# Optimization experiments

Measured on AMD Instinct MI355X. Metric: run time of the kernel, lower is better.

Reference implementation:

```python
import jax, jax.numpy as jnp
import numpy as np

N_EMBD = 1024
N_HEAD = 16
HEAD_SIZE = 64
EPS = 1e-5


def _layer_norm(x, gamma, beta, eps=EPS):
    mu = jnp.mean(x, axis=-1, keepdims=True)
    var = jnp.mean(jnp.square(x - mu), axis=-1, keepdims=True)
    return (x - mu) * jax.lax.rsqrt(var + eps) * gamma + beta


def setup_inputs() -> dict:
    key = jax.random.key(0)
    ks = jax.random.split(key, 10)
    C = N_EMBD
    s = 1.0 / np.sqrt(C)
    x = jax.random.normal(ks[0], (4, 2048, C), dtype=jnp.float32)
    Wq = jax.random.normal(ks[1], (C, C), dtype=jnp.float32) * s
    Wk = jax.random.normal(ks[2], (C, C), dtype=jnp.float32) * s
    Wv = jax.random.normal(ks[3], (C, C), dtype=jnp.float32) * s
    Wo = jax.random.normal(ks[4], (C, C), dtype=jnp.float32) * s
    W1 = jax.random.normal(ks[5], (C, 4 * C), dtype=jnp.float32) * s
    b1 = jnp.zeros((4 * C,), dtype=jnp.float32)
    W2 = jax.random.normal(ks[6], (4 * C, C), dtype=jnp.float32) * (1.0 / np.sqrt(4 * C))
    b2 = jnp.zeros((C,), dtype=jnp.float32)
    g1 = jnp.ones((C,), dtype=jnp.float32)
    be1 = jnp.zeros((C,), dtype=jnp.float32)
    g2 = jnp.ones((C,), dtype=jnp.float32)
    be2 = jnp.zeros((C,), dtype=jnp.float32)
    return {"x": x, "Wq": Wq, "Wk": Wk, "Wv": Wv, "Wo": Wo,
            "W1": W1, "b1": b1, "W2": W2, "b2": b2,
            "g1": g1, "be1": be1, "g2": g2, "be2": be2}


def _block(x, Wq, Wk, Wv, Wo, W1, b1, W2, b2, g1, be1, g2, be2):
    B, T, C = x.shape
    H, D = N_HEAD, HEAD_SIZE
    # attention sub-block
    h = _layer_norm(x, g1, be1)
    q = (h @ Wq.T).reshape(B, T, H, D).transpose(0, 2, 1, 3)  # [B,H,T,D]
    k = (h @ Wk.T).reshape(B, T, H, D).transpose(0, 2, 1, 3)
    v = (h @ Wv.T).reshape(B, T, H, D).transpose(0, 2, 1, 3)
    wei = jnp.einsum("bhqd,bhkd->bhqk", q, k) * (D ** -0.5)
    causal = jnp.tril(jnp.ones((T, T), dtype=bool))
    wei = jnp.where(causal, wei, -jnp.inf)
    wei = jax.nn.softmax(wei, axis=-1)
    out = jnp.einsum("bhqk,bhkd->bhqd", wei, v)
    out = out.transpose(0, 2, 1, 3).reshape(B, T, C)
    x = x + out @ Wo.T
    # FFN sub-block (exact erf GELU, matching torch default)
    h2 = _layer_norm(x, g2, be2)
    ff = jax.nn.gelu(h2 @ W1 + b1, approximate=False) @ W2 + b2
    return x + ff


def reference(x, Wq, Wk, Wv, Wo, W1, b1, W2, b2, g1, be1, g2, be2):
    return _block(x, Wq, Wk, Wv, Wo, W1, b1, W2, b2, g1, be1, g2, be2)
```

## Files before the change

kernel.cpp:

```cpp
#include <hip/hip_runtime.h>
#include <cmath>

typedef unsigned short u16;
typedef __attribute__((ext_vector_type(8))) short bf16x8;
typedef __attribute__((ext_vector_type(4))) float f32x4;

#define TT 2048
#define CC 1024
#define BT 8192

__device__ __forceinline__ u16 f2bf(float f) {
  unsigned u = __builtin_bit_cast(unsigned, f);
  u += 0x7fffu + ((u >> 16) & 1u);
  return (u16)(u >> 16);
}

__device__ __forceinline__ float bf2f(u16 u) {
  return __builtin_bit_cast(float, (unsigned)u << 16);
}

__device__ __forceinline__ float gelu_tanh(float v) {
  float u2 = v * (1.595769122f + 0.071354816f * v * v);
  return v / (1.f + __expf(-u2));
}

__device__ __forceinline__ void gload_lds16(const void* g, void* l) {
  __builtin_amdgcn_global_load_lds(
      (const __attribute__((address_space(1))) void*)g,
      (__attribute__((address_space(3))) void*)l, 16, 0, 0);
}


__global__ __launch_bounds__(256) void cvt_kernel(const float* __restrict__ s,
                                                  u16* __restrict__ d) {
  int i = (blockIdx.x * 256 + threadIdx.x) * 4;
  float4 v = *(const float4*)(s + i);
  ushort4 o;
  o.x = f2bf(v.x); o.y = f2bf(v.y); o.z = f2bf(v.z); o.w = f2bf(v.w);
  *(ushort4*)(d + i) = o;
}

__global__ __launch_bounds__(256) void transpose_cvt(const float* __restrict__ src,
                                                     u16* __restrict__ dst,
                                                     int R, int C) {
  __shared__ float tile[32][33];
  int c0 = blockIdx.x * 32, r0 = blockIdx.y * 32;
  int tx = threadIdx.x, ty = threadIdx.y;
#pragma unroll
  for (int j = 0; j < 4; ++j)
    tile[ty + j * 8][tx] = src[(size_t)(r0 + ty + j * 8) * C + c0 + tx];
  __syncthreads();
#pragma unroll
  for (int j = 0; j < 4; ++j)
    dst[(size_t)(c0 + ty + j * 8) * R + r0 + tx] = f2bf(tile[tx][ty + j * 8]);
}


__global__ __launch_bounds__(256) void ln_kernel(const float* __restrict__ x,
                                                 const float* __restrict__ gw,
                                                 const float* __restrict__ bw,
                                                 u16* __restrict__ out) {
  int row = blockIdx.x;
  int tid = threadIdx.x;
  const size_t base = (size_t)row * CC;
  float4 v = *(const float4*)(x + base + tid * 4);
  float s = v.x + v.y + v.z + v.w;
  float q = v.x * v.x + v.y * v.y + v.z * v.z + v.w * v.w;
#pragma unroll
  for (int o = 32; o > 0; o >>= 1) {
    s += __shfl_down(s, o, 64);
    q += __shfl_down(q, o, 64);
  }
  __shared__ float red[8];
  __shared__ float stat[2];
  int lane = tid & 63, wid = tid >> 6;
  if (!lane) { red[wid] = s; red[4 + wid] = q; }
  __syncthreads();
  if (!tid) {
    float S = red[0] + red[1] + red[2] + red[3];
    float Q = red[4] + red[5] + red[6] + red[7];
    float mu = S * (1.0f / CC);
    float var = Q * (1.0f / CC) - mu * mu;
    stat[0] = mu;
    stat[1] = rsqrtf(var + 1e-5f);
  }
  __syncthreads();
  float mu = stat[0], rs = stat[1];
  int c = tid * 4;
  float4 gv = *(const float4*)(gw + c);
  float4 bv = *(const float4*)(bw + c);
  ushort4 o;
  o.x = f2bf((v.x - mu) * rs * gv.x + bv.x);
  o.y = f2bf((v.y - mu) * rs * gv.y + bv.y);
  o.z = f2bf((v.z - mu) * rs * gv.z + bv.z);
  o.w = f2bf((v.w - mu) * rs * gv.w + bv.w);
  *(ushort4*)(out + base + c) = o;
}


__global__ __launch_bounds__(256) void rf2_kernel(const u16* __restrict__ p0,
                                                  const u16* __restrict__ p1,
                                                  const float* __restrict__ b2,
                                                  const float* __restrict__ resid,
                                                  float* __restrict__ out) {
  int c = threadIdx.x * 4;
  size_t i = (size_t)blockIdx.x * CC + c;
  ushort4 a = *(const ushort4*)(p0 + i);
  ushort4 b = *(const ushort4*)(p1 + i);
  float4 r = *(const float4*)(resid + i);
  float4 bb = *(const float4*)(b2 + c);
  float4 o;
  o.x = bf2f(a.x) + bf2f(b.x) + r.x + bb.x;
  o.y = bf2f(a.y) + bf2f(b.y) + r.y + bb.y;
  o.z = bf2f(a.z) + bf2f(b.z) + r.z + bb.z;
  o.w = bf2f(a.w) + bf2f(b.w) + r.w + bb.w;
  *(float4*)(out + i) = o;
}


template <int EPI>
__global__ __launch_bounds__(512) void gemm256(const u16* __restrict__ A,
                                               const u16* __restrict__ B,
                                               void* __restrict__ Cv,
                                               const float* __restrict__ bias,
                                               const float* __restrict__ resid,
                                               u16* __restrict__ vt,
                                               int N, int K, int Kst,
                                               int gn, int kdiv) {
  __shared__ u16 lds[8][8192];
  const int tid = threadIdx.x, lane = tid & 63, wid = tid >> 6;
  const int nwg = gridDim.x;
  const int bid = blockIdx.x;
  const int sb = (nwg & 7) ? bid : ((bid & 7) * (nwg >> 3) + (bid >> 3));
  const int kslice = sb / kdiv, rem = sb % kdiv;
  const int tM = (rem / gn) * 256, tN = (rem % gn) * 256;
  const int wm = wid >> 2, wn = wid & 3;
  const int fr = lane & 15, g4 = lane >> 4;
  const int gsw = (g4 ^ ((fr >> 3) << 1)) * 8;
  const int srow0 = wid * 16 + (lane >> 2);
  const int scol = ((lane & 3) ^ ((lane >> 5) << 1)) * 8;
  const u16* pA = A + (size_t)kslice * K + (size_t)tM * Kst + (size_t)srow0 * Kst + scol;
  const u16* pB = B + (size_t)kslice * K + (size_t)tN * Kst + (size_t)srow0 * Kst + scol;
  const int NKT = K >> 6;
  f32x4 acc[8][4] = {};

  auto stage = [&](int idx) {
    int kof = (idx >> 1) << 5;
    const u16* G = (idx & 1) ? pB : pA;
    u16* dst = &lds[idx & 7][wid * 512];
    gload_lds16(G + kof, dst);
    gload_lds16(G + (size_t)128 * Kst + kof, dst + 4096);
  };

#pragma unroll
  for (int j = 0; j < 4; ++j) stage(j);
  asm volatile("s_waitcnt vmcnt(4)" ::: "memory");
#pragma unroll
  for (int j = 4; j < 7; ++j) stage(j);
  asm volatile("s_waitcnt vmcnt(6)" ::: "memory");
  __builtin_amdgcn_s_barrier();

  for (int t2 = 0; t2 < NKT; t2 += 2) {
#pragma unroll
    for (int tt = 0; tt < 2; ++tt) {
      const int t = t2 + tt;
      const int bo = tt << 2;
#pragma unroll
      for (int ks = 0; ks < 2; ++ks) {
        const u16* Ah = lds[bo | (ks << 1)];
        const u16* Bh = lds[bo | (ks << 1) | 1];
        bf16x8 bfr[4];
#pragma unroll
        for (int ni = 0; ni < 4; ++ni)
          bfr[ni] = *(const bf16x8*)&Bh[(wn * 64 + ni * 16 + fr) * 32 + gsw];
#pragma unroll
        for (int mh = 0; mh < 2; ++mh) {
          bf16x8 af[4];
#pragma unroll
          for (int mi = 0; mi < 4; ++mi)
            af[mi] = *(const bf16x8*)&Ah[(wm * 128 + mh * 64 + mi * 16 + fr) * 32 + gsw];
          __builtin_amdgcn_sched_barrier(0);
          int idx = 4 * t + (ks << 1) + mh + 7;
          if (idx < 4 * NKT) stage(idx);
          __builtin_amdgcn_s_barrier();
          asm volatile("s_waitcnt lgkmcnt(0)" ::: "memory");
          __builtin_amdgcn_sched_barrier(0);
          __builtin_amdgcn_s_setprio(1);
#pragma unroll
          for (int mi = 0; mi < 4; ++mi)
#pragma unroll
            for (int ni = 0; ni < 4; ++ni)
              acc[mh * 4 + mi][ni] = __builtin_amdgcn_mfma_f32_16x16x32_bf16(
                  af[mi], bfr[ni], acc[mh * 4 + mi][ni], 0, 0, 0);
          __builtin_amdgcn_s_setprio(0);
          __builtin_amdgcn_sched_barrier(0);
          if (ks == 1 && mh == 1) {
            if (t < NKT - 2) asm volatile("s_waitcnt vmcnt(6)" ::: "memory");
            else if (t == NKT - 2) asm volatile("s_waitcnt vmcnt(0)" ::: "memory");
          }
          __builtin_amdgcn_s_barrier();
        }
      }
    }
  }

#pragma unroll
  for (int m = 0; m < 8; ++m) {
#pragma unroll
    for (int ni = 0; ni < 4; ++ni) {
      const int gR0 = tM + wm * 128 + m * 16 + g4 * 4;
      const int gC = tN + wn * 64 + ni * 16 + fr;
      if constexpr (EPI == 4) {
        if (gC < 2048) {
          float sc = (gC < 1024) ? 0.125f : 1.0f;
#pragma unroll
          for (int r = 0; r < 4; ++r)
            ((u16*)Cv)[(size_t)(gR0 + r) * 3072 + gC] = f2bf(acc[m][ni][r] * sc);
        } else {
          int tr = gR0 & 2047, bb = gR0 >> 11;
          int dv = gC - 2048, hh = dv >> 6, dd = dv & 63;
          int k5 = tr & 31;
          int pos = ((k5 & 15) >> 2) * 8 + ((k5 >> 4) & 1) * 4;
          ushort4 q4;
          q4.x = f2bf(acc[m][ni][0]);
          q4.y = f2bf(acc[m][ni][1]);
          q4.z = f2bf(acc[m][ni][2]);
          q4.w = f2bf(acc[m][ni][3]);
          *(ushort4*)&vt[((size_t)((bb * 16 + hh) * 64 + dd)) * 2048 + (tr & ~31) + pos] = q4;
        }
      } else if constexpr (EPI == 0) {
        u16* dst = kslice ? vt : (u16*)Cv;
#pragma unroll
        for (int r = 0; r < 4; ++r)
          dst[(size_t)(gR0 + r) * N + gC] = f2bf(acc[m][ni][r]);
      } else if constexpr (EPI == 2) {
#pragma unroll
        for (int r = 0; r < 4; ++r) {
          float v = gelu_tanh(acc[m][ni][r] + bias[gC]);
          ((u16*)Cv)[(size_t)(gR0 + r) * N + gC] = f2bf(v);
        }
      } else {
#pragma unroll
        for (int r = 0; r < 4; ++r) {
          size_t idx = (size_t)(gR0 + r) * N + gC;
          float v = acc[m][ni][r] + resid[idx];
          if constexpr (EPI == 3) v += bias[gC];
          ((float*)Cv)[idx] = v;
        }
      }
    }
  }
}


__global__ __launch_bounds__(256) void attn_kernel(const u16* __restrict__ qkv,
                                                   const u16* __restrict__ vt,
                                                   u16* __restrict__ out) {
  const int pair = blockIdx.x;
  const int bh = blockIdx.y;
  const int b = bh >> 4, h = bh & 15;
  const int tid = threadIdx.x, lane = tid & 63, wid = tid >> 6;
  const int ql = lane & 15, g = lane >> 4;
  const int sw = ql & 7;
  __shared__ u16 Ks[2][4096];
  __shared__ u16 Vs[2][4096];
  const size_t rowQbase = (size_t)b * TT;
  const u16* kpart = qkv + rowQbase * 3072 + 1024 + h * 64;
  const u16* vpart = vt + ((size_t)(b * 16 + h) * 64) * 2048;
  const int srow = lane >> 3;
  const int sc16 = lane & 7;

  for (int pass = 0; pass < 2; ++pass) {
    const int qt = pass ? (31 - pair) : pair;
    const int qrow0 = qt * 64 + wid * 16;
    const int q_glb = qrow0 + ql;
    const u16* qp = qkv + (rowQbase + q_glb) * 3072 + h * 64 + g * 8;
    bf16x8 qf0 = *(const bf16x8*)qp;
    bf16x8 qf1 = *(const bf16x8*)(qp + 32);
    f32x4 o[4] = {};
    float m_run = -1e30f, l_run = 0.f;
    const int nt = qt + 1;

    auto stage = [&](int bufi, int t) {
      int kv0 = t * 64;
#pragma unroll
      for (int i = 0; i < 2; ++i) {
        int seg = wid * 2 + i;
        int rloc = seg * 8 + srow;
        int cs = (sc16 ^ (rloc & 7)) * 8;
        gload_lds16(kpart + (size_t)(kv0 + rloc) * 3072 + cs, &Ks[bufi][seg * 512]);
        gload_lds16(vpart + (size_t)rloc * 2048 + kv0 + cs, &Vs[bufi][seg * 512]);
      }
    };

    stage(0, 0);
    __syncthreads();
    int buf = 0;
    for (int t = 0; t < nt; ++t) {
      if (t + 1 < nt) stage(buf ^ 1, t + 1);
      const u16* Kb = Ks[buf];
      const u16* Vb = Vs[buf];
      const int kv0 = t * 64;
      float p[16];
#pragma unroll
      for (int kt = 0; kt < 4; ++kt) {
        int row = kt * 16 + ql;
        bf16x8 k0 = *(const bf16x8*)&Kb[row * 64 + ((g ^ sw) * 8)];
        bf16x8 k1 = *(const bf16x8*)&Kb[row * 64 + (((4 + g) ^ sw) * 8)];
        f32x4 s = {0.f, 0.f, 0.f, 0.f};
        s = __builtin_amdgcn_mfma_f32_16x16x32_bf16(k0, qf0, s, 0, 0, 0);
        s = __builtin_amdgcn_mfma_f32_16x16x32_bf16(k1, qf1, s, 0, 0, 0);
        if (t == qt) {
#pragma unroll
          for (int r = 0; r < 4; ++r) {
            int k_glb = kv0 + kt * 16 + 4 * g + r;
            p[kt * 4 + r] = (k_glb <= q_glb) ? s[r] : -1e30f;
          }
        } else {
#pragma unroll
          for (int r = 0; r < 4; ++r) p[kt * 4 + r] = s[r];
        }
      }
      float mloc = p[0];
#pragma unroll
      for (int i = 1; i < 16; ++i) mloc = fmaxf(mloc, p[i]);
      mloc = fmaxf(mloc, __shfl_xor(mloc, 16));
      mloc = fmaxf(mloc, __shfl_xor(mloc, 32));
      float mnew = fmaxf(m_run, mloc);
      float alpha = __expf(m_run - mnew);
      float lloc = 0.f;
      bf16x8 pa0, pa1;
#pragma unroll
      for (int i = 0; i < 16; ++i) {
        float e = __expf(p[i] - mnew);
        lloc += e;
        if (i < 8) pa0[i] = (short)f2bf(e);
        else pa1[i - 8] = (short)f2bf(e);
      }
      lloc += __shfl_xor(lloc, 16);
      lloc += __shfl_xor(lloc, 32);
      l_run = l_run * alpha + lloc;
      m_run = mnew;
      float aO[4];
#pragma unroll
      for (int r = 0; r < 4; ++r) aO[r] = __shfl(alpha, 4 * g + r);
#pragma unroll
      for (int d0 = 0; d0 < 4; ++d0) {
#pragma unroll
        for (int r = 0; r < 4; ++r) o[d0][r] *= aO[r];
      }
#pragma unroll
      for (int d0 = 0; d0 < 4; ++d0) {
        int row = d0 * 16 + ql;
        bf16x8 v0 = *(const bf16x8*)&Vb[row * 64 + ((g ^ sw) * 8)];
        bf16x8 v1 = *(const bf16x8*)&Vb[row * 64 + (((4 + g) ^ sw) * 8)];
        o[d0] = __builtin_amdgcn_mfma_f32_16x16x32_bf16(pa0, v0, o[d0], 0, 0, 0);
        o[d0] = __builtin_amdgcn_mfma_f32_16x16x32_bf16(pa1, v1, o[d0], 0, 0, 0);
      }
      __syncthreads();
      buf ^= 1;
    }
    float linv = 1.0f / l_run;
    float lO[4];
#pragma unroll
    for (int r = 0; r < 4; ++r) lO[r] = __shfl(linv, 4 * g + r);
#pragma unroll
    for (int d0 = 0; d0 < 4; ++d0) {
#pragma unroll
      for (int r = 0; r < 4; ++r) {
        size_t idx = (rowQbase + qrow0 + 4 * g + r) * CC + h * 64 + d0 * 16 + ql;
        out[idx] = f2bf(o[d0][r] * lO[r]);
      }
    }
  }
}


extern "C" void kernel_launch(void* const* d_in, const int* in_sizes, int n_in,
                              void* d_out, int out_size, void* d_ws, size_t ws_size,
                              hipStream_t stream) {
  const float* x   = (const float*)d_in[0];
  const float* Wq  = (const float*)d_in[1];
  const float* Wk  = (const float*)d_in[2];
  const float* Wv  = (const float*)d_in[3];
  const float* Wo  = (const float*)d_in[4];
  const float* W1  = (const float*)d_in[5];
  const float* b1  = (const float*)d_in[6];
  const float* W2  = (const float*)d_in[7];
  const float* b2  = (const float*)d_in[8];
  const float* g1  = (const float*)d_in[9];
  const float* be1 = (const float*)d_in[10];
  const float* g2  = (const float*)d_in[11];
  const float* be2 = (const float*)d_in[12];

  char* ws = (char*)d_ws;
  size_t off = 0;
  u16* Wqkv = (u16*)(ws + off); off += (size_t)3072 * 1024 * 2;
  u16* Wob  = (u16*)(ws + off); off += (size_t)1024 * 1024 * 2;
  u16* W1T  = (u16*)(ws + off); off += (size_t)4096 * 1024 * 2;
  u16* W2T  = (u16*)(ws + off); off += (size_t)1024 * 4096 * 2;
  u16* Hb   = (u16*)(ws + off); off += (size_t)BT * 1024 * 2;
  u16* QKV  = (u16*)(ws + off); off += (size_t)BT * 3072 * 2;
  u16* AttO = (u16*)(ws + off); off += (size_t)BT * 1024 * 2;
  float* X2 = (float*)(ws + off); off += (size_t)BT * 1024 * 4;
  u16* FF1 = QKV;
  u16* VT  = (u16*)X2;
  if (ws_size < off) return;
  const int KBIG = 1 << 20;

  cvt_kernel<<<1024, 256, 0, stream>>>(Wq, Wqkv);
  cvt_kernel<<<1024, 256, 0, stream>>>(Wk, Wqkv + 1024 * 1024);
  cvt_kernel<<<1024, 256, 0, stream>>>(Wv, Wqkv + 2 * 1024 * 1024);
  cvt_kernel<<<1024, 256, 0, stream>>>(Wo, Wob);
  transpose_cvt<<<dim3(128, 32), dim3(32, 8), 0, stream>>>(W1, W1T, 1024, 4096);
  transpose_cvt<<<dim3(32, 128), dim3(32, 8), 0, stream>>>(W2, W2T, 4096, 1024);

  ln_kernel<<<BT, 256, 0, stream>>>(x, g1, be1, Hb);
  gemm256<4><<<32 * 12, 512, 0, stream>>>(Hb, Wqkv, QKV, nullptr, nullptr, VT,
                                          3072, 1024, 1024, 12, KBIG);
  attn_kernel<<<dim3(16, 64), 256, 0, stream>>>(QKV, VT, AttO);
  gemm256<1><<<32 * 4, 512, 0, stream>>>(AttO, Wob, X2, nullptr, x, nullptr,
                                         1024, 1024, 1024, 4, KBIG);
  ln_kernel<<<BT, 256, 0, stream>>>(X2, g2, be2, Hb);
  gemm256<2><<<32 * 16, 512, 0, stream>>>(Hb, W1T, FF1, b1, nullptr, nullptr,
                                          4096, 1024, 1024, 16, KBIG);
  gemm256<0><<<32 * 8, 512, 0, stream>>>(FF1, W2T, Hb, nullptr, nullptr, AttO,
                                         1024, 2048, 4096, 4, 128);
  rf2_kernel<<<BT, 256, 0, stream>>>(Hb, AttO, b2, X2, (float*)d_out);
}
```

Measured before the change: 407.3 us.

## Rework attention softmax with exp2, lazy rescale, packed bf16 and block swizzle

Folds log2(e) into the Q scale so softmax can use the native exp2 instruction. The running-max rescale of the output accumulator is skipped unless some row's max grows by more than 8. The conversion to bf16 now uses packed hardware instructions, and the max and sum reductions are written as trees. MFMA sections are wrapped in s_setprio, and the attention grid is flattened to 1D with a swizzle that spreads heads across XCDs. Together these aim to cut VALU work in the softmax; the lazy rescale adds some numerical risk if exponents grow large.

```diff
diff --git a/kernel.cpp b/kernel.cpp
--- a/kernel.cpp
+++ b/kernel.cpp
@@ -8,6 +8,10 @@
 #define TT 2048
 #define CC 1024
 #define BT 8192
+
+__device__ __forceinline__ float fexp2(float x) {
+  return __builtin_amdgcn_exp2f(x);
+}
 
 __device__ __forceinline__ u16 f2bf(float f) {
   unsigned u = __builtin_bit_cast(unsigned, f);
@@ -212,7 +216,7 @@
       const int gC = tN + wn * 64 + ni * 16 + fr;
       if constexpr (EPI == 4) {
         if (gC < 2048) {
-          float sc = (gC < 1024) ? 0.125f : 1.0f;
+          float sc = (gC < 1024) ? 0.180336884f : 1.0f;
 #pragma unroll
           for (int r = 0; r < 4; ++r)
             ((u16*)Cv)[(size_t)(gR0 + r) * 3072 + gC] = f2bf(acc[m][ni][r] * sc);
@@ -256,8 +260,10 @@
 __global__ __launch_bounds__(256) void attn_kernel(const u16* __restrict__ qkv,
                                                    const u16* __restrict__ vt,
                                                    u16* __restrict__ out) {
-  const int pair = blockIdx.x;
-  const int bh = blockIdx.y;
+  const int bid = blockIdx.x;
+  const int sb = (bid & 7) * 128 + (bid >> 3);
+  const int pair = sb & 15;
+  const int bh = sb >> 4;
   const int b = bh >> 4, h = bh & 15;
   const int tid = threadIdx.x, lane = tid & 63, wid = tid >> 6;
   const int ql = lane & 15, g = lane >> 4;
@@ -302,6 +308,7 @@
       const u16* Vb = Vs[buf];
       const int kv0 = t * 64;
       float p[16];
+      __builtin_amdgcn_s_setprio(1);
 #pragma unroll
       for (int kt = 0; kt < 4; ++kt) {
         int row = kt * 16 + ql;
@@ -321,34 +328,52 @@
           for (int r = 0; r < 4; ++r) p[kt * 4 + r] = s[r];
         }
       }
-      float mloc = p[0];
-#pragma unroll
-      for (int i = 1; i < 16; ++i) mloc = fmaxf(mloc, p[i]);
+      __builtin_amdgcn_s_setprio(0);
+      float t8[8];
+#pragma unroll
+      for (int i = 0; i < 8; ++i) t8[i] = fmaxf(p[i], p[i + 8]);
+#pragma unroll
+      for (int i = 0; i < 4; ++i) t8[i] = fmaxf(t8[i], t8[i + 4]);
+      float mloc = fmaxf(fmaxf(t8[0], t8[1]), fmaxf(t8[2], t8[3]));
       mloc = fmaxf(mloc, __shfl_xor(mloc, 16));
       mloc = fmaxf(mloc, __shfl_xor(mloc, 32));
-      float mnew = fmaxf(m_run, mloc);
-      float alpha = __expf(m_run - mnew);
-      float lloc = 0.f;
-      bf16x8 pa0, pa1;
-#pragma unroll
-      for (int i = 0; i < 16; ++i) {
-        float e = __expf(p[i] - mnew);
-        lloc += e;
-        if (i < 8) pa0[i] = (short)f2bf(e);
-        else pa1[i - 8] = (short)f2bf(e);
-      }
+      if (!__all(mloc <= m_run + 8.f)) {
+        float mnew = fmaxf(m_run, mloc);
+        float alpha = fexp2(m_run - mnew);
+        m_run = mnew;
+        l_run *= alpha;
+        float aO[4];
+#pragma unroll
+        for (int r = 0; r < 4; ++r) aO[r] = __shfl(alpha, 4 * g + r);
+#pragma unroll
+        for (int d0 = 0; d0 < 4; ++d0)
+#pragma unroll
+          for (int r = 0; r < 4; ++r) o[d0][r] *= aO[r];
+      }
+      float e[16];
+#pragma unroll
+      for (int i = 0; i < 16; ++i) e[i] = fexp2(p[i] - m_run);
+      float s8[8];
+#pragma unroll
+      for (int i = 0; i < 8; ++i) s8[i] = e[i] + e[i + 8];
+#pragma unroll
+      for (int i = 0; i < 4; ++i) s8[i] += s8[i + 4];
+      float lloc = (s8[0] + s8[1]) + (s8[2] + s8[3]);
       lloc += __shfl_xor(lloc, 16);
       lloc += __shfl_xor(lloc, 32);
-      l_run = l_run * alpha + lloc;
-      m_run = mnew;
-      float aO[4];
-#pragma unroll
-      for (int r = 0; r < 4; ++r) aO[r] = __shfl(alpha, 4 * g + r);
-#pragma unroll
-      for (int d0 = 0; d0 < 4; ++d0) {
-#pragma unroll
-        for (int r = 0; r < 4; ++r) o[d0][r] *= aO[r];
-      }
+      l_run += lloc;
+      int4 w0, w1;
+      asm("v_cvt_pk_bf16_f32 %0, %1, %2" : "=v"(w0.x) : "v"(e[0]), "v"(e[1]));
+      asm("v_cvt_pk_bf16_f32 %0, %1, %2" : "=v"(w0.y) : "v"(e[2]), "v"(e[3]));
+      asm("v_cvt_pk_bf16_f32 %0, %1, %2" : "=v"(w0.z) : "v"(e[4]), "v"(e[5]));
+      asm("v_cvt_pk_bf16_f32 %0, %1, %2" : "=v"(w0.w) : "v"(e[6]), "v"(e[7]));
+      asm("v_cvt_pk_bf16_f32 %0, %1, %2" : "=v"(w1.x) : "v"(e[8]), "v"(e[9]));
+      asm("v_cvt_pk_bf16_f32 %0, %1, %2" : "=v"(w1.y) : "v"(e[10]), "v"(e[11]));
+      asm("v_cvt_pk_bf16_f32 %0, %1, %2" : "=v"(w1.z) : "v"(e[12]), "v"(e[13]));
+      asm("v_cvt_pk_bf16_f32 %0, %1, %2" : "=v"(w1.w) : "v"(e[14]), "v"(e[15]));
+      bf16x8 pa0 = __builtin_bit_cast(bf16x8, w0);
+      bf16x8 pa1 = __builtin_bit_cast(bf16x8, w1);
+      __builtin_amdgcn_s_setprio(1);
 #pragma unroll
       for (int d0 = 0; d0 < 4; ++d0) {
         int row = d0 * 16 + ql;
@@ -357,6 +382,7 @@
         o[d0] = __builtin_amdgcn_mfma_f32_16x16x32_bf16(pa0, v0, o[d0], 0, 0, 0);
         o[d0] = __builtin_amdgcn_mfma_f32_16x16x32_bf16(pa1, v1, o[d0], 0, 0, 0);
       }
+      __builtin_amdgcn_s_setprio(0);
       __syncthreads();
       buf ^= 1;
     }
@@ -418,7 +444,7 @@
   ln_kernel<<<BT, 256, 0, stream>>>(x, g1, be1, Hb);
   gemm256<4><<<32 * 12, 512, 0, stream>>>(Hb, Wqkv, QKV, nullptr, nullptr, VT,
                                           3072, 1024, 1024, 12, KBIG);
-  attn_kernel<<<dim3(16, 64), 256, 0, stream>>>(QKV, VT, AttO);
+  attn_kernel<<<1024, 256, 0, stream>>>(QKV, VT, AttO);
   gemm256<1><<<32 * 4, 512, 0, stream>>>(AttO, Wob, X2, nullptr, x, nullptr,
                                          1024, 1024, 1024, 4, KBIG);
   ln_kernel<<<BT, 256, 0, stream>>>(X2, g2, be2, Hb);
```

After: 389.8 us. 1.04x faster.
